# Kernel optimization log

Hardware: AMD Instinct MI355X
Metric: run time of the kernel (lower is better)

The kernel has to match this reference:

```python
import jax, jax.numpy as jnp
import numpy as np

BIT = 8      # shared-exponent mantissa bits (bf_conf.*_bit)
GSZ = 36     # block size (bf_conf.*_sz)


def bfp_quantize(x, bit=BIT, sz=GSZ):
    """Block floating point: groups of `sz` consecutive elements share one
    exponent e = floor(log2(max|x|)); each element keeps `bit` mantissa bits."""
    shape = x.shape
    flat = x.reshape(-1)
    n = flat.shape[0]
    pad = (-n) % sz
    flat = jnp.pad(flat, (0, pad))
    g = flat.reshape(-1, sz)                                   # [G, sz]
    maxabs = jnp.max(jnp.abs(g), axis=1, keepdims=True)
    e = jnp.floor(jnp.log2(jnp.where(maxabs > 0, maxabs, 1.0)))
    scale = jnp.exp2(e - (bit - 1))                            # lsb of shared-exp format
    q = jnp.round(g / scale) * scale
    q = jnp.where(maxabs > 0, q, 0.0)
    return q.reshape(-1)[:n].reshape(shape)


def setup_inputs() -> dict:
    key = jax.random.key(0)
    k1, k2, k3 = jax.random.split(key, 3)
    B, Cin, Cout, H, W, K = 16, 32, 32, 224, 224, 3
    x = jax.random.normal(k1, (B, Cin, H, W), dtype=jnp.float32)
    fan_in = Cin * K * K
    bound = 1.0 / np.sqrt(fan_in)
    weight = jax.random.uniform(k2, (Cout, Cin, K, K), jnp.float32, -bound, bound)
    bias = jax.random.uniform(k3, (Cout,), jnp.float32, -bound, bound)
    return {"x": x, "weight": weight, "bias": bias}


def reference(x, weight, bias):
    xq = bfp_quantize(x)          # f_i
    wq = bfp_quantize(weight)     # f_w
    out = jax.lax.conv_general_dilated(
        xq, wq,
        window_strides=(1, 1),
        padding=((1, 1), (1, 1)),
        rhs_dilation=(1, 1),
        feature_group_count=1,
        dimension_numbers=("NCHW", "OIHW", "NCHW"),
    )
    out = out + bias[None, :, None, None]
    out = bfp_quantize(out)       # f_o
    return out
```

## Files before the change

### kernel.cpp

```cpp
#include <hip/hip_runtime.h>
#include <hip/hip_bf16.h>

#define GSZ 36
static const int NX  = 16 * 32 * 224 * 224;
static const int NX4 = NX / 4;
static const int NW  = 32 * 32 * 3 * 3;
static const int GXN = (NX + GSZ - 1) / GSZ;
static const int HWp = 224 * 224;
static const int NBOUND = NX / 448;

typedef short bf16x8 __attribute__((ext_vector_type(8)));
typedef float f32x4  __attribute__((ext_vector_type(4)));

__device__ __forceinline__ unsigned div36(unsigned n) {
    return (unsigned)(((unsigned long long)n * 954437177ull) >> 35);
}
__device__ __forceinline__ float scale_from_max(float m) {
    int e = (int)((__float_as_uint(m) >> 23) & 0xffu) - 127;
    return __uint_as_float((unsigned)(e + 120) << 23);
}
__device__ __forceinline__ float inv_from_scale(float s) {
    return __uint_as_float(0x7F000000u - __float_as_uint(s));
}
__device__ __forceinline__ unsigned short f2bf(float f) {
    return (unsigned short)(__float_as_uint(f) >> 16);
}
__device__ __forceinline__ float bf2f(unsigned short u) {
    return __uint_as_float(((unsigned)u) << 16);
}

__global__ void k_quant_wt(const float* __restrict__ w, unsigned short* __restrict__ wt) {
    int g = threadIdx.x;
    int base = g * GSZ;
    float v[GSZ];
    const float4* p = reinterpret_cast<const float4*>(w + base);
    #pragma unroll
    for (int i = 0; i < 9; ++i) {
        float4 t = p[i];
        v[4*i+0] = t.x; v[4*i+1] = t.y; v[4*i+2] = t.z; v[4*i+3] = t.w;
    }
    float m = 0.0f;
    #pragma unroll
    for (int i = 0; i < GSZ; ++i) m = fmaxf(m, fabsf(v[i]));
    if (m > 0.0f) {
        float s = scale_from_max(m), inv = inv_from_scale(s);
        #pragma unroll
        for (int i = 0; i < GSZ; ++i) v[i] = rintf(v[i] * inv) * s;
    }
    #pragma unroll
    for (int i = 0; i < GSZ; ++i) {
        int f = base + i;
        int co = f / 288, rem = f - co * 288;
        int ci = rem / 9, s = rem - ci * 9;
        wt[s * 1024 + co * 32 + ci] = f2bf(v[i]);
    }
}

#define TSTR 452
__global__ __launch_bounds__(256, 4) void k_quant_x_fused(const float* __restrict__ x,
                                                          unsigned short* __restrict__ xt) {
    __shared__ unsigned short tile[32 * TSTR];
    __shared__ float scl[32 * 14];
    __shared__ int rem36s[32], offs[32];

    int t = threadIdx.x;
    int b = blockIdx.y, hp = blockIdx.x;
    int F0 = (b * 32) * HWp + hp * 448;

    if (t < 32) {
        int F = F0 + t * HWp;
        int r = F - 36 * (int)div36((unsigned)F);
        rem36s[t] = r;
        offs[t] = (F - r) & 3;
    }
    for (int i = t; i < 448; i += 256) ((unsigned*)scl)[i] = 0u;
    __syncthreads();

    for (int j = 0; j < 16; ++j) {
        int idx = t + 256 * j;
        int ci = idx >> 7, c4 = idx & 127;
        int off = offs[ci];
        int base4 = F0 + ci * HWp - rem36s[ci] - off;
        int f4 = (base4 >> 2) + c4;
        float4 v = make_float4(0.f, 0.f, 0.f, 0.f);
        if ((unsigned)f4 < (unsigned)NX4)
            v = reinterpret_cast<const float4*>(x)[f4];
        int rel0 = 4 * c4 - off;
        int r0c = rel0 > 0 ? rel0 : 0;
        int gia = (int)div36((unsigned)r0c);
        int bnd = 36 * gia + 36;
        float av[4] = {fabsf(v.x), fabsf(v.y), fabsf(v.z), fabsf(v.w)};
        float ma = 0.f, mb = 0.f;
        #pragma unroll
        for (int k = 0; k < 4; ++k) {
            int rel = rel0 + k;
            float a = ((unsigned)rel < 504u) ? av[k] : 0.f;
            if (rel < bnd) ma = fmaxf(ma, a); else mb = fmaxf(mb, a);
        }
        if (ma > 0.f) atomicMax((unsigned*)&scl[ci * 14 + gia], __float_as_uint(ma));
        if (mb > 0.f) atomicMax((unsigned*)&scl[ci * 14 + gia + 1], __float_as_uint(mb));
    }
    __syncthreads();
    for (int i = t; i < 448; i += 256)
        scl[i] = scale_from_max(__uint_as_float(((unsigned*)scl)[i]));
    __syncthreads();

    for (int j = 0; j < 14; ++j) {
        int eidx = t + 256 * j;
        int ci = ((eidx >> 4) * 293) >> 11;
        int c4 = eidx - ci * 112;
        float4 v = reinterpret_cast<const float4*>(x)[((F0 + ci * HWp) >> 2) + c4];
        int rbase = rem36s[ci] + 4 * c4;
        int gi0 = (int)div36((unsigned)rbase);
        int rr = rbase - 36 * gi0;
        float vv[4] = {v.x, v.y, v.z, v.w};
        unsigned short qb[4];
        #pragma unroll
        for (int k = 0; k < 4; ++k) {
            int gi = gi0 + ((rr + k) >= 36 ? 1 : 0);
            float s = scl[ci * 14 + gi];
            qb[k] = f2bf(rintf(vv[k] * inv_from_scale(s)) * s);
        }
        uint2 o;
        o.x = (unsigned)qb[0] | ((unsigned)qb[1] << 16);
        o.y = (unsigned)qb[2] | ((unsigned)qb[3] << 16);
        *reinterpret_cast<uint2*>(&tile[ci * TSTR + 4 * c4]) = o;
    }
    __syncthreads();

    unsigned short* ob = xt + ((size_t)b * HWp + hp * 448) * 32;
    for (int j = 0; j < 7; ++j) {
        int qd = t + 256 * j;
        int px = qd >> 2;
        int c0 = (qd & 3) * 8;
        unsigned uu[4];
        #pragma unroll
        for (int p = 0; p < 4; ++p) {
            unsigned short lo = tile[(c0 + 2 * p) * TSTR + px];
            unsigned short hi = tile[(c0 + 2 * p + 1) * TSTR + px];
            uu[p] = (unsigned)lo | ((unsigned)hi << 16);
        }
        *reinterpret_cast<uint4*>(ob + (size_t)px * 32 + c0) =
            make_uint4(uu[0], uu[1], uu[2], uu[3]);
    }
}

__global__ __launch_bounds__(512, 4) void k_conv_fused(const unsigned short* __restrict__ xt,
                                                       const unsigned short* __restrict__ wt,
                                                       const float* __restrict__ bias,
                                                       float* __restrict__ out) {
    __shared__ __align__(16) unsigned short smem[4 * 226 * 40];

    int tid  = threadIdx.x;
    int lane = tid & 63;
    int wid  = tid >> 6;
    int j = blockIdx.x;
    int b = blockIdx.y;
    int h0 = j * 2;

    const unsigned short* xb = xt + (size_t)b * HWp * 32;
    #pragma unroll
    for (int it = 0; it < 8; ++it) {
        int q = tid + it * 512;
        if (q < 3616) {
            int r = q / 904, rem = q - r * 904;
            int px = rem >> 2, c = rem & 3;
            int gh = h0 - 1 + r, gw = px - 1;
            uint4 val = make_uint4(0u, 0u, 0u, 0u);
            if ((unsigned)gh < 224u && (unsigned)gw < 224u)
                val = *reinterpret_cast<const uint4*>(xb + ((size_t)(gh * 224 + gw)) * 32 + c * 8);
            *reinterpret_cast<uint4*>(&smem[(r * 226 + px) * 40 + c * 8]) = val;
        }
    }

    int row = wid >> 2, cohalf = (wid >> 1) & 1, phalf = wid & 1;
    int m = lane & 15, kg = lane >> 4;
    int m4 = kg << 2;

    bf16x8 Wf[9];
    #pragma unroll
    for (int s = 0; s < 9; ++s)
        Wf[s] = *reinterpret_cast<const bf16x8*>(
            wt + s * 1024 + (cohalf * 16 + m) * 32 + kg * 8);

    f32x4 binit;
    #pragma unroll
    for (int r4 = 0; r4 < 4; ++r4) binit[r4] = bias[cohalf * 16 + m4 + r4];
    f32x4 acc[7];
    #pragma unroll
    for (int g = 0; g < 7; ++g) acc[g] = binit;

    __syncthreads();

    #pragma unroll
    for (int s = 0; s < 9; ++s) {
        int kh = s / 3, kw = s - kh * 3;
        int rbase = (row + kh) * 226;
        #pragma unroll
        for (int g = 0; g < 7; ++g) {
            int px = phalf * 112 + g * 16 + m + kw;
            bf16x8 X = *reinterpret_cast<const bf16x8*>(&smem[(rbase + px) * 40 + kg * 8]);
            acc[g] = __builtin_amdgcn_mfma_f32_16x16x32_bf16(Wf[s], X, acc[g], 0, 0, 0);
        }
    }

    __syncthreads();

    unsigned short* obuf = smem;
    float* scl = reinterpret_cast<float*>(smem + 14336);

    #pragma unroll
    for (int g = 0; g < 7; ++g) {
        int rp = row * 224 + phalf * 112 + g * 16 + m;
        #pragma unroll
        for (int r4 = 0; r4 < 4; ++r4) {
            int co = cohalf * 16 + m4 + r4;
            obuf[co * 448 + rp] = f2bf(acc[g][r4]);
        }
    }
    __syncthreads();

    if (tid < 384) {
        int co = tid / 12, tt = tid - 12 * (tid / 12);
        int M = 112 * (b * 32 + co) + j;
        int s36 = (16 * M) % 36;
        int head = (36 - s36) % 36;
        int ninter = (448 - head) / 36;
        if (tt < ninter) {
            int base = co * 448 + head + 36 * tt;
            float mx = 0.f;
            #pragma unroll
            for (int k = 0; k < 36; ++k) mx = fmaxf(mx, fabsf(bf2f(obuf[base + k])));
            scl[co * 12 + tt] = (mx > 0.f) ? scale_from_max(mx) : 0.f;
        }
    }
    __syncthreads();

    int head4[4], tail4[4], co4[4];
    #pragma unroll
    for (int r4 = 0; r4 < 4; ++r4) {
        int co = cohalf * 16 + m4 + r4;
        co4[r4] = co;
        int M = 112 * (b * 32 + co) + j;
        int s36 = (16 * M) % 36;
        int head = (36 - s36) % 36;
        head4[r4] = head;
        tail4[r4] = head + 36 * ((448 - head) / 36);
    }
    #pragma unroll
    for (int g = 0; g < 7; ++g) {
        int wl = phalf * 112 + g * 16 + m;
        int rp = row * 224 + wl;
        #pragma unroll
        for (int r4 = 0; r4 < 4; ++r4) {
            float v = acc[g][r4];
            if (rp >= head4[r4] && rp < tail4[r4]) {
                int t36 = (rp - head4[r4]) / 36;
                float s = scl[co4[r4] * 12 + t36];
                if (s != 0.f) v = rintf(v * inv_from_scale(s)) * s;
            }
            out[((size_t)(b * 32 + co4[r4]) * 224 + (h0 + row)) * 224 + wl] = v;
        }
    }
}

__global__ __launch_bounds__(256) void k_fixup(float* __restrict__ out) {
    int gw = (int)((blockIdx.x * 256 + threadIdx.x) >> 6);
    int lane = threadIdx.x & 63;
    int mIdx = gw + 1;
    if (mIdx >= NBOUND) return;
    if (mIdx % 9 == 0) return;
    int f = 448 * mIdx;
    int base = 36 * (int)div36((unsigned)f);
    float v = 0.f;
    if (lane < 36) v = out[base + lane];
    float a = fabsf(v);
    #pragma unroll
    for (int d = 1; d < 64; d <<= 1) a = fmaxf(a, __shfl_xor(a, d));
    if (lane < 36 && a > 0.f) {
        float s = scale_from_max(a);
        out[base + lane] = rintf(v * inv_from_scale(s)) * s;
    }
}

extern "C" void kernel_launch(void* const* d_in, const int* in_sizes, int n_in,
                              void* d_out, int out_size, void* d_ws, size_t ws_size,
                              hipStream_t stream) {
    (void)in_sizes; (void)n_in; (void)out_size; (void)ws_size;
    const float* x    = (const float*)d_in[0];
    const float* w    = (const float*)d_in[1];
    const float* bias = (const float*)d_in[2];
    float* out        = (float*)d_out;

    unsigned short* xt = (unsigned short*)d_ws;
    unsigned short* wt = xt + NX;

    k_quant_wt<<<1, 256, 0, stream>>>(w, wt);
    k_quant_x_fused<<<dim3(112, 16), 256, 0, stream>>>(x, xt);
    k_conv_fused<<<dim3(112, 16), 512, 0, stream>>>(xt, wt, bias, out);
    k_fixup<<<(NBOUND - 1 + 3) / 4, 256, 0, stream>>>(out);
}
```

Measured before the change: 265.0 us.

## Fold weight quantization into x-quant launch and stage boundary groups in side buffer

Weight quantization now runs in an extra block column of the x-quantization kernel, which drops one launch. The conv kernel writes the unquantized values of straddling boundary groups to a side buffer, so the fixup kernel reads them from contiguous memory instead of reloading from the output. The shared output staging buffer gets a padded stride to cut bank conflicts, and the per-group max is now taken on packed 32-bit pairs. The alignment offset handling in x-quant is also dropped. The extra side-buffer writes add some global traffic.

```diff
diff --git a/kernel.cpp b/kernel.cpp
--- a/kernel.cpp
+++ b/kernel.cpp
@@ -5,7 +5,6 @@
 static const int NX  = 16 * 32 * 224 * 224;
 static const int NX4 = NX / 4;
 static const int NW  = 32 * 32 * 3 * 3;
-static const int GXN = (NX + GSZ - 1) / GSZ;
 static const int HWp = 224 * 224;
 static const int NBOUND = NX / 448;
 
@@ -29,49 +28,50 @@
     return __uint_as_float(((unsigned)u) << 16);
 }
 
-__global__ void k_quant_wt(const float* __restrict__ w, unsigned short* __restrict__ wt) {
-    int g = threadIdx.x;
-    int base = g * GSZ;
-    float v[GSZ];
-    const float4* p = reinterpret_cast<const float4*>(w + base);
-    #pragma unroll
-    for (int i = 0; i < 9; ++i) {
-        float4 t = p[i];
-        v[4*i+0] = t.x; v[4*i+1] = t.y; v[4*i+2] = t.z; v[4*i+3] = t.w;
-    }
-    float m = 0.0f;
-    #pragma unroll
-    for (int i = 0; i < GSZ; ++i) m = fmaxf(m, fabsf(v[i]));
-    if (m > 0.0f) {
-        float s = scale_from_max(m), inv = inv_from_scale(s);
-        #pragma unroll
-        for (int i = 0; i < GSZ; ++i) v[i] = rintf(v[i] * inv) * s;
-    }
-    #pragma unroll
-    for (int i = 0; i < GSZ; ++i) {
-        int f = base + i;
-        int co = f / 288, rem = f - co * 288;
-        int ci = rem / 9, s = rem - ci * 9;
-        wt[s * 1024 + co * 32 + ci] = f2bf(v[i]);
-    }
-}
-
 #define TSTR 452
-__global__ __launch_bounds__(256, 4) void k_quant_x_fused(const float* __restrict__ x,
-                                                          unsigned short* __restrict__ xt) {
+__global__ __launch_bounds__(256, 4) void k_quant_x(const float* __restrict__ x,
+                                                    unsigned short* __restrict__ xt,
+                                                    const float* __restrict__ w,
+                                                    unsigned short* __restrict__ wtq) {
     __shared__ unsigned short tile[32 * TSTR];
     __shared__ float scl[32 * 14];
-    __shared__ int rem36s[32], offs[32];
+    __shared__ int rem36s[32];
 
     int t = threadIdx.x;
-    int b = blockIdx.y, hp = blockIdx.x;
+    int hp = blockIdx.x, b = blockIdx.y;
+
+    if (hp == 112) {
+        if (b != 0) return;
+        int base = t * GSZ;
+        float v[GSZ];
+        const float4* p = reinterpret_cast<const float4*>(w + base);
+        #pragma unroll
+        for (int i = 0; i < 9; ++i) {
+            float4 q = p[i];
+            v[4*i+0] = q.x; v[4*i+1] = q.y; v[4*i+2] = q.z; v[4*i+3] = q.w;
+        }
+        float m = 0.0f;
+        #pragma unroll
+        for (int i = 0; i < GSZ; ++i) m = fmaxf(m, fabsf(v[i]));
+        if (m > 0.0f) {
+            float s = scale_from_max(m), inv = inv_from_scale(s);
+            #pragma unroll
+            for (int i = 0; i < GSZ; ++i) v[i] = rintf(v[i] * inv) * s;
+        }
+        #pragma unroll
+        for (int i = 0; i < GSZ; ++i) {
+            int f = base + i;
+            int co = f / 288, rem = f - co * 288;
+            int ci = rem / 9, s = rem - ci * 9;
+            wtq[s * 1024 + co * 32 + ci] = f2bf(v[i]);
+        }
+        return;
+    }
+
     int F0 = (b * 32) * HWp + hp * 448;
-
     if (t < 32) {
         int F = F0 + t * HWp;
-        int r = F - 36 * (int)div36((unsigned)F);
-        rem36s[t] = r;
-        offs[t] = (F - r) & 3;
+        rem36s[t] = F - 36 * (int)div36((unsigned)F);
     }
     for (int i = t; i < 448; i += 256) ((unsigned*)scl)[i] = 0u;
     __syncthreads();
@@ -79,15 +79,13 @@
     for (int j = 0; j < 16; ++j) {
         int idx = t + 256 * j;
         int ci = idx >> 7, c4 = idx & 127;
-        int off = offs[ci];
-        int base4 = F0 + ci * HWp - rem36s[ci] - off;
+        int base4 = F0 + ci * HWp - rem36s[ci];
         int f4 = (base4 >> 2) + c4;
         float4 v = make_float4(0.f, 0.f, 0.f, 0.f);
         if ((unsigned)f4 < (unsigned)NX4)
             v = reinterpret_cast<const float4*>(x)[f4];
-        int rel0 = 4 * c4 - off;
-        int r0c = rel0 > 0 ? rel0 : 0;
-        int gia = (int)div36((unsigned)r0c);
+        int rel0 = 4 * c4;
+        int gia = (int)div36((unsigned)rel0);
         int bnd = 36 * gia + 36;
         float av[4] = {fabsf(v.x), fabsf(v.y), fabsf(v.z), fabsf(v.w)};
         float ma = 0.f, mb = 0.f;
@@ -145,10 +143,12 @@
     }
 }
 
+#define OBS 450
 __global__ __launch_bounds__(512, 4) void k_conv_fused(const unsigned short* __restrict__ xt,
                                                        const unsigned short* __restrict__ wt,
                                                        const float* __restrict__ bias,
-                                                       float* __restrict__ out) {
+                                                       float* __restrict__ out,
+                                                       float* __restrict__ side) {
     __shared__ __align__(16) unsigned short smem[4 * 226 * 40];
 
     int tid  = threadIdx.x;
@@ -205,44 +205,49 @@
     }
 
     __syncthreads();
-
     unsigned short* obuf = smem;
-    float* scl = reinterpret_cast<float*>(smem + 14336);
+    float* scl = reinterpret_cast<float*>(smem + 32 * OBS);
 
     #pragma unroll
     for (int g = 0; g < 7; ++g) {
         int rp = row * 224 + phalf * 112 + g * 16 + m;
         #pragma unroll
-        for (int r4 = 0; r4 < 4; ++r4) {
-            int co = cohalf * 16 + m4 + r4;
-            obuf[co * 448 + rp] = f2bf(acc[g][r4]);
-        }
+        for (int r4 = 0; r4 < 4; ++r4)
+            obuf[(cohalf * 16 + m4 + r4) * OBS + rp] = f2bf(acc[g][r4]);
     }
     __syncthreads();
 
     if (tid < 384) {
         int co = tid / 12, tt = tid - 12 * (tid / 12);
         int M = 112 * (b * 32 + co) + j;
-        int s36 = (16 * M) % 36;
+        int s36 = (16 * (M % 9)) % 36;
         int head = (36 - s36) % 36;
         int ninter = (448 - head) / 36;
         if (tt < ninter) {
-            int base = co * 448 + head + 36 * tt;
+            const unsigned* p32 = reinterpret_cast<const unsigned*>(obuf);
+            int idx = co * (OBS / 2) + (head >> 1) + 18 * tt;
             float mx = 0.f;
             #pragma unroll
-            for (int k = 0; k < 36; ++k) mx = fmaxf(mx, fabsf(bf2f(obuf[base + k])));
+            for (int k = 0; k < 18; ++k) {
+                unsigned a = p32[idx + k] & 0x7fff7fffu;
+                mx = fmaxf(mx, fmaxf(__uint_as_float(a << 16),
+                                     __uint_as_float(a & 0xffff0000u)));
+            }
             scl[co * 12 + tt] = (mx > 0.f) ? scale_from_max(mx) : 0.f;
         }
     }
     __syncthreads();
 
-    int head4[4], tail4[4], co4[4];
+    int M4a[4], head4[4], tail4[4], s364[4], s36p4[4], co4[4];
     #pragma unroll
     for (int r4 = 0; r4 < 4; ++r4) {
         int co = cohalf * 16 + m4 + r4;
         co4[r4] = co;
         int M = 112 * (b * 32 + co) + j;
-        int s36 = (16 * M) % 36;
+        M4a[r4] = M;
+        int s36 = (16 * (M % 9)) % 36;
+        s364[r4] = s36;
+        s36p4[r4] = (s36 + 16) % 36;
         int head = (36 - s36) % 36;
         head4[r4] = head;
         tail4[r4] = head + 36 * ((448 - head) / 36);
@@ -254,8 +259,12 @@
         #pragma unroll
         for (int r4 = 0; r4 < 4; ++r4) {
             float v = acc[g][r4];
-            if (rp >= head4[r4] && rp < tail4[r4]) {
-                int t36 = (rp - head4[r4]) / 36;
+            if (rp < head4[r4]) {
+                side[36 * M4a[r4] + s364[r4] + rp] = v;
+            } else if (rp >= tail4[r4]) {
+                side[36 * (M4a[r4] + 1) + rp - 448 + s36p4[r4]] = v;
+            } else {
+                int t36 = (int)div36((unsigned)(rp - head4[r4]));
                 float s = scl[co4[r4] * 12 + t36];
                 if (s != 0.f) v = rintf(v * inv_from_scale(s)) * s;
             }
@@ -264,22 +273,25 @@
     }
 }
 
-__global__ __launch_bounds__(256) void k_fixup(float* __restrict__ out) {
+__global__ __launch_bounds__(256) void k_fixup(const float* __restrict__ side,
+                                               float* __restrict__ out) {
     int gw = (int)((blockIdx.x * 256 + threadIdx.x) >> 6);
     int lane = threadIdx.x & 63;
     int mIdx = gw + 1;
-    if (mIdx >= NBOUND) return;
-    if (mIdx % 9 == 0) return;
-    int f = 448 * mIdx;
-    int base = 36 * (int)div36((unsigned)f);
+    if (mIdx > NBOUND) return;
+    int u9 = mIdx % 9;
+    if (u9 == 0) return;
+    int s36 = (16 * u9) % 36;
+    int G = 448 * mIdx - s36;
+    int cnt = NX - G; if (cnt > 36) cnt = 36;
     float v = 0.f;
-    if (lane < 36) v = out[base + lane];
+    if (lane < cnt) v = side[36 * mIdx + lane];
     float a = fabsf(v);
     #pragma unroll
     for (int d = 1; d < 64; d <<= 1) a = fmaxf(a, __shfl_xor(a, d));
-    if (lane < 36 && a > 0.f) {
+    if (lane < cnt && a > 0.f) {
         float s = scale_from_max(a);
-        out[base + lane] = rintf(v * inv_from_scale(s)) * s;
+        out[G + lane] = rintf(v * inv_from_scale(s)) * s;
     }
 }
 
@@ -294,9 +306,9 @@
 
     unsigned short* xt = (unsigned short*)d_ws;
     unsigned short* wt = xt + NX;
-
-    k_quant_wt<<<1, 256, 0, stream>>>(w, wt);
-    k_quant_x_fused<<<dim3(112, 16), 256, 0, stream>>>(x, xt);
-    k_conv_fused<<<dim3(112, 16), 512, 0, stream>>>(xt, wt, bias, out);
-    k_fixup<<<(NBOUND - 1 + 3) / 4, 256, 0, stream>>>(out);
-}
+    float* side = (float*)(wt + NW);
+
+    k_quant_x<<<dim3(113, 16), 256, 0, stream>>>(x, xt, w, wt);
+    k_conv_fused<<<dim3(112, 16), 512, 0, stream>>>(xt, wt, bias, out, side);
+    k_fixup<<<(NBOUND + 3) / 4, 256, 0, stream>>>(side, out);
+}
```

New measurement: 275.8 us. 4.1% more time.
